# Performance work log

Measured on AMD Instinct MI355X. Metric: run time of the kernel, lower is better.

The kernel has to match this reference:

```python
import jax, jax.numpy as jnp
import numpy as np

NUM_NODES = 100000
EMB = 64
HID = 128
OUT = 64
N_EDGES = 1600000
N_LABEL = 200000


def setup_inputs() -> dict:
    key = jax.random.key(0)
    ks = jax.random.split(key, 8)
    return {
        "emb": jax.random.normal(ks[0], (NUM_NODES, EMB), jnp.float32) * 0.05,
        "w1l": jax.random.normal(ks[1], (HID, EMB), jnp.float32) * 0.05,
        "w1r": jax.random.normal(ks[2], (HID, EMB), jnp.float32) * 0.05,
        "b1": jnp.zeros((HID,), jnp.float32),
        "w2l": jax.random.normal(ks[3], (OUT, HID), jnp.float32) * 0.05,
        "w2r": jax.random.normal(ks[4], (OUT, HID), jnp.float32) * 0.05,
        "b2": jnp.zeros((OUT,), jnp.float32),
        "edge_index": jax.random.randint(ks[5], (2, N_EDGES), 0, NUM_NODES, jnp.int32),
        "edge_label_index": jax.random.randint(ks[6], (2, N_LABEL), 0, NUM_NODES, jnp.int32),
    }


def reference(emb, w1l, w1r, b1, w2l, w2r, b2, edge_index, edge_label_index):
    # PyG SAGEConv (aggr='mean'): out = mean_{j in N(i)} x_j @ W_l^T + b_l + x_i @ W_r^T
    n = emb.shape[0]
    src, dst = edge_index[0], edge_index[1]
    # in-degree per destination node, clamped to avoid div-by-zero (isolated nodes -> 0 agg)
    deg = jax.ops.segment_sum(jnp.ones(src.shape, emb.dtype), dst, num_segments=n)
    inv_deg = 1.0 / jnp.maximum(deg, 1.0)

    def sage(x, wl, wr, b):
        agg = jax.ops.segment_sum(x[src], dst, num_segments=n) * inv_deg[:, None]
        return agg @ wl.T + x @ wr.T + b

    h = jax.nn.relu(sage(emb, w1l, w1r, b1))  # dropout is identity in eval mode
    z = sage(h, w2l, w2r, b2)  # [N, OUT]
    # dot-product decode over candidate pairs
    return jnp.sum(z[edge_label_index[0]] * z[edge_label_index[1]], axis=-1)
```

## Files before the change

### kernel.cpp

```cpp
#include <hip/hip_runtime.h>

#define NN   100000
#define EMB  64
#define HID  128
#define OUTD 64
#define NE   1600000
#define NL   200000
#define NBUK 6250
#define NG   8
#define CAPG 128
#define BSTR 6272

typedef __attribute__((ext_vector_type(4))) float f32x4;
typedef __attribute__((ext_vector_type(8))) short s16x8;
typedef __attribute__((ext_vector_type(4))) unsigned short us4;

__device__ __forceinline__ unsigned short f2bf(float f) {
    unsigned u = __float_as_uint(f);
    u += 0x7FFFu + ((u >> 16) & 1u);
    return (unsigned short)(u >> 16);
}
__device__ __forceinline__ float bf2f(unsigned short h) {
    return __uint_as_float(((unsigned)h) << 16);
}

__device__ __forceinline__ unsigned xcc_id() {
    unsigned v;
    asm volatile("s_getreg_b32 %0, hwreg(HW_REG_XCC_ID)" : "=s"(v));
    return v & (NG - 1);
}

__global__ void bucket16_kernel(const int* __restrict__ src, const int* __restrict__ dst,
                                int* __restrict__ bcnt, int* __restrict__ tmp) {
    int i = blockIdx.x * blockDim.x + threadIdx.x;
    if (i >= NE / 4) return;
    unsigned g = xcc_id();
    int* cb = bcnt + g * BSTR;
    int4 d4 = ((const int4*)dst)[i];
    int4 s4 = ((const int4*)src)[i];
    int b0 = d4.x >> 4, b1 = d4.y >> 4, b2 = d4.z >> 4, b3 = d4.w >> 4;
    int p0 = atomicAdd(&cb[b0], 1);
    int p1 = atomicAdd(&cb[b1], 1);
    int p2 = atomicAdd(&cb[b2], 1);
    int p3 = atomicAdd(&cb[b3], 1);
    if (p0 < CAPG) tmp[((size_t)g * NBUK + b0) * CAPG + p0] = ((d4.x & 15) << 17) | s4.x;
    if (p1 < CAPG) tmp[((size_t)g * NBUK + b1) * CAPG + p1] = ((d4.y & 15) << 17) | s4.y;
    if (p2 < CAPG) tmp[((size_t)g * NBUK + b2) * CAPG + p2] = ((d4.z & 15) << 17) | s4.z;
    if (p3 < CAPG) tmp[((size_t)g * NBUK + b3) * CAPG + p3] = ((d4.w & 15) << 17) | s4.w;
}

__global__ void conv_emb_kernel(const float* __restrict__ emb, unsigned short* __restrict__ embb) {
    int i = blockIdx.x * blockDim.x + threadIdx.x;
    if (i >= NN * 16) return;
    float4 v = ((const float4*)emb)[i];
    us4 o;
    o.x = f2bf(v.x); o.y = f2bf(v.y); o.z = f2bf(v.z); o.w = f2bf(v.w);
    ((us4*)embb)[i] = o;
}

__global__ void conv_w_kernel(const float* __restrict__ w1l, const float* __restrict__ w1r,
                              const float* __restrict__ w2l, const float* __restrict__ w2r,
                              unsigned short* __restrict__ w1cat, unsigned short* __restrict__ w2cat) {
    int t = blockIdx.x * blockDim.x + threadIdx.x;
    if (t >= 128 * 128) return;
    int o = t >> 7, k = t & 127;
    w1cat[t] = f2bf(k < 64 ? w1l[o * 64 + k] : w1r[o * 64 + (k - 64)]);
    w2cat[t] = f2bf(o < 64 ? w2l[o * 128 + k] : w2r[(o - 64) * 128 + k]);
}

template<bool L1>
__global__ void __launch_bounds__(256) agg16_kernel(
        const int* __restrict__ bcnt, const int* __restrict__ tmp,
        const unsigned short* __restrict__ xb,
        const float* __restrict__ hz, const float* __restrict__ bias,
        unsigned short* __restrict__ outb, float* __restrict__ outf) {
    __shared__ int cgs[NG];
    __shared__ int goff[NG];
    __shared__ int total;
    __shared__ int scnt[16];
    __shared__ int soff[16];
    __shared__ int scur[16];
    __shared__ int plist[NG * CAPG];
    __shared__ int slist[NG * CAPG];

    const int b    = blockIdx.x;
    const int tid  = threadIdx.x;
    const int lane = tid & 63;
    const int wv   = tid >> 6;

    if (tid < NG) cgs[tid] = min(bcnt[tid * BSTR + b], CAPG);
    if (tid < 16) scnt[tid] = 0;
    __syncthreads();

    if (tid == 0) {
        int acc = 0;
#pragma unroll
        for (int g = 0; g < NG; ++g) { int c = cgs[g]; goff[g] = acc; acc += c; }
        total = acc;
    }
    __syncthreads();

    for (int t = tid; t < NG * CAPG; t += 256) {
        int g = t >> 7;
        int i = t & (CAPG - 1);
        if (i < cgs[g])
            plist[goff[g] + i] = tmp[((size_t)g * NBUK + b) * CAPG + i];
    }
    __syncthreads();

    const int cnt = total;
    for (int i = tid; i < cnt; i += 256)
        atomicAdd(&scnt[plist[i] >> 17], 1);
    __syncthreads();

    if (tid == 0) {
        int acc = 0;
#pragma unroll
        for (int r = 0; r < 16; ++r) {
            soff[r] = acc;
            scur[r] = acc;
            acc += scnt[r];
        }
    }
    __syncthreads();

    for (int i = tid; i < cnt; i += 256) {
        int p = plist[i];
        int pos = atomicAdd(&scur[p >> 17], 1);
        slist[pos] = p & 0x1FFFF;
    }
    __syncthreads();

#define LDX(c) bf2f(xb[(size_t)(c) * 64 + lane])
    for (int r = wv; r < 16; r += 4) {
        const int node = b * 16 + r;
        const int s = soff[r];
        const int d = scnt[r];
        float acc = 0.f;
        int j = 0;
        for (; j + 8 <= d; j += 8) {
            int c0 = slist[s + j + 0], c1 = slist[s + j + 1];
            int c2 = slist[s + j + 2], c3 = slist[s + j + 3];
            int c4 = slist[s + j + 4], c5 = slist[s + j + 5];
            int c6 = slist[s + j + 6], c7 = slist[s + j + 7];
            float v0 = LDX(c0), v1 = LDX(c1), v2 = LDX(c2), v3 = LDX(c3);
            float v4 = LDX(c4), v5 = LDX(c5), v6 = LDX(c6), v7 = LDX(c7);
            acc += ((v0 + v1) + (v2 + v3)) + ((v4 + v5) + (v6 + v7));
        }
        if (j + 4 <= d) {
            int c0 = slist[s + j + 0], c1 = slist[s + j + 1];
            int c2 = slist[s + j + 2], c3 = slist[s + j + 3];
            float v0 = LDX(c0), v1 = LDX(c1), v2 = LDX(c2), v3 = LDX(c3);
            acc += (v0 + v1) + (v2 + v3);
            j += 4;
        }
        for (; j < d; ++j) acc += LDX(slist[s + j]);

        const float inv = 1.0f / fmaxf((float)d, 1.0f);
        if (L1) {
            outb[(size_t)node * 64 + lane] = f2bf(acc * inv);
        } else {
            outf[(size_t)node * 64 + lane] =
                acc * inv + hz[(size_t)node * 64 + lane] + bias[lane];
        }
    }
#undef LDX
}

__global__ void __launch_bounds__(256) gemm_mfma_kernel(
        const unsigned short* __restrict__ aggb, const unsigned short* __restrict__ embb,
        const unsigned short* __restrict__ w1cat, const float* __restrict__ b1,
        const unsigned short* __restrict__ w2cat,
        unsigned short* __restrict__ p2b, float* __restrict__ hz) {
    __shared__ unsigned short h_lds[128 * 136];

    const int tid  = threadIdx.x;
    const int lane = tid & 63;
    const int w    = tid >> 6;
    const int l15  = lane & 15;
    const int lk   = lane >> 4;
    const int n_base = blockIdx.x * 128;
    const int mrow0  = w * 32;

    f32x4 acc[2][8];
#pragma unroll
    for (int mt = 0; mt < 2; ++mt)
#pragma unroll
        for (int nt = 0; nt < 8; ++nt) acc[mt][nt] = (f32x4)(0.f);

#pragma unroll
    for (int ks = 0; ks < 4; ++ks) {
        const int kc = ks * 32 + lk * 8;
        s16x8 a[2];
#pragma unroll
        for (int mt = 0; mt < 2; ++mt) {
            int n = n_base + mrow0 + mt * 16 + l15;
            s16x8 av = (s16x8)(short)0;
            if (n < NN) {
                const unsigned short* ap = (kc < 64)
                    ? (aggb + (size_t)n * 64 + kc)
                    : (embb + (size_t)n * 64 + (kc - 64));
                av = *(const s16x8*)ap;
            }
            a[mt] = av;
        }
#pragma unroll
        for (int nt = 0; nt < 8; ++nt) {
            s16x8 bv = *(const s16x8*)(w1cat + (nt * 16 + l15) * 128 + kc);
            acc[0][nt] = __builtin_amdgcn_mfma_f32_16x16x32_bf16(a[0], bv, acc[0][nt], 0, 0, 0);
            acc[1][nt] = __builtin_amdgcn_mfma_f32_16x16x32_bf16(a[1], bv, acc[1][nt], 0, 0, 0);
        }
    }

    float b1v[8];
#pragma unroll
    for (int nt = 0; nt < 8; ++nt) b1v[nt] = b1[nt * 16 + l15];
#pragma unroll
    for (int mt = 0; mt < 2; ++mt)
#pragma unroll
        for (int nt = 0; nt < 8; ++nt) {
            f32x4 d = acc[mt][nt];
            int o = nt * 16 + l15;
            int r0 = mrow0 + mt * 16 + lk * 4;
#pragma unroll
            for (int j = 0; j < 4; ++j)
                h_lds[(r0 + j) * 136 + o] = f2bf(fmaxf(d[j] + b1v[nt], 0.f));
        }

#pragma unroll
    for (int mt = 0; mt < 2; ++mt)
#pragma unroll
        for (int nt = 0; nt < 8; ++nt) acc[mt][nt] = (f32x4)(0.f);

#pragma unroll
    for (int ks = 0; ks < 4; ++ks) {
        const int kc = ks * 32 + lk * 8;
        s16x8 a[2];
#pragma unroll
        for (int mt = 0; mt < 2; ++mt)
            a[mt] = *(const s16x8*)&h_lds[(mrow0 + mt * 16 + l15) * 136 + kc];
#pragma unroll
        for (int nt = 0; nt < 8; ++nt) {
            s16x8 bv = *(const s16x8*)(w2cat + (nt * 16 + l15) * 128 + kc);
            acc[0][nt] = __builtin_amdgcn_mfma_f32_16x16x32_bf16(a[0], bv, acc[0][nt], 0, 0, 0);
            acc[1][nt] = __builtin_amdgcn_mfma_f32_16x16x32_bf16(a[1], bv, acc[1][nt], 0, 0, 0);
        }
    }

#pragma unroll
    for (int mt = 0; mt < 2; ++mt)
#pragma unroll
        for (int nt = 0; nt < 8; ++nt) {
            f32x4 d = acc[mt][nt];
            int o = nt * 16 + l15;
            int r0 = n_base + mrow0 + mt * 16 + lk * 4;
#pragma unroll
            for (int j = 0; j < 4; ++j) {
                int r = r0 + j;
                if (r >= NN) continue;
                if (nt < 4) p2b[(size_t)r * 64 + o] = f2bf(d[j]);
                else        hz[(size_t)r * 64 + (o - 64)] = d[j];
            }
        }
}

__global__ void decode_kernel(const int* __restrict__ a, const int* __restrict__ b,
                              const float* __restrict__ z, float* __restrict__ out) {
    int t = blockIdx.x * blockDim.x + threadIdx.x;
    int k = t >> 4;
    int q = t & 15;
    if (k >= NL) return;
    int ia = a[k], ib = b[k];
    float4 va = ((const float4*)z)[ia * 16 + q];
    float4 vb = ((const float4*)z)[ib * 16 + q];
    float s = va.x * vb.x + va.y * vb.y + va.z * vb.z + va.w * vb.w;
    s += __shfl_xor(s, 1, 64);
    s += __shfl_xor(s, 2, 64);
    s += __shfl_xor(s, 4, 64);
    s += __shfl_xor(s, 8, 64);
    if (q == 0) out[k] = s;
}

extern "C" void kernel_launch(void* const* d_in, const int* in_sizes, int n_in,
                              void* d_out, int out_size, void* d_ws, size_t ws_size,
                              hipStream_t stream) {
    const float* emb = (const float*)d_in[0];
    const float* w1l = (const float*)d_in[1];
    const float* w1r = (const float*)d_in[2];
    const float* b1  = (const float*)d_in[3];
    const float* w2l = (const float*)d_in[4];
    const float* w2r = (const float*)d_in[5];
    const float* b2  = (const float*)d_in[6];
    const int*   ei  = (const int*)d_in[7];
    const int*   eli = (const int*)d_in[8];
    float* out = (float*)d_out;

    int* bcnt = (int*)d_ws;
    int* tmp  = bcnt + NG * BSTR;
    unsigned short* aggb  = (unsigned short*)(tmp + (size_t)NG * NBUK * CAPG);
    unsigned short* embb  = aggb + (size_t)NN * 64;
    unsigned short* p2b   = embb + (size_t)NN * 64;
    unsigned short* w1cat = p2b + (size_t)NN * 64;
    unsigned short* w2cat = w1cat + 128 * 128;
    float* hz = (float*)(w2cat + 128 * 128);
    float* z  = hz + (size_t)NN * 64;

    const int* src = ei;
    const int* dst = ei + NE;

    hipMemsetAsync(bcnt, 0, (size_t)NG * BSTR * sizeof(int), stream);

    bucket16_kernel<<<(NE / 4 + 255) / 256, 256, 0, stream>>>(src, dst, bcnt, tmp);
    conv_emb_kernel<<<(NN * 16 + 255) / 256, 256, 0, stream>>>(emb, embb);
    conv_w_kernel<<<64, 256, 0, stream>>>(w1l, w1r, w2l, w2r, w1cat, w2cat);

    agg16_kernel<true><<<NBUK, 256, 0, stream>>>(bcnt, tmp, embb, nullptr, nullptr,
                                                 aggb, nullptr);

    const int NT = (NN + 127) / 128;
    gemm_mfma_kernel<<<NT, 256, 0, stream>>>(aggb, embb, w1cat, b1, w2cat, p2b, hz);

    agg16_kernel<false><<<NBUK, 256, 0, stream>>>(bcnt, tmp, p2b, hz, b2,
                                                  nullptr, z);

    decode_kernel<<<(NL * 16 + 255) / 256, 256, 0, stream>>>(eli, eli + NL, z, out);
}
```

Measured before the change: 237.2 us.

## Fuse prep kernels, store final z in bf16, use nontemporal loads

```diff
diff --git a/kernel.cpp b/kernel.cpp
--- a/kernel.cpp
+++ b/kernel.cpp
@@ -11,9 +11,14 @@
 #define CAPG 128
 #define BSTR 6272
 
+#define BUK_BLOCKS  1563
+#define CEMB_BLOCKS 400
+#define CW_BLOCKS   64
+
 typedef __attribute__((ext_vector_type(4))) float f32x4;
 typedef __attribute__((ext_vector_type(8))) short s16x8;
 typedef __attribute__((ext_vector_type(4))) unsigned short us4;
+typedef __attribute__((ext_vector_type(4))) int v4i;
 
 __device__ __forceinline__ unsigned short f2bf(float f) {
     unsigned u = __float_as_uint(f);
@@ -30,42 +35,46 @@
     return v & (NG - 1);
 }
 
-__global__ void bucket16_kernel(const int* __restrict__ src, const int* __restrict__ dst,
-                                int* __restrict__ bcnt, int* __restrict__ tmp) {
-    int i = blockIdx.x * blockDim.x + threadIdx.x;
-    if (i >= NE / 4) return;
-    unsigned g = xcc_id();
-    int* cb = bcnt + g * BSTR;
-    int4 d4 = ((const int4*)dst)[i];
-    int4 s4 = ((const int4*)src)[i];
-    int b0 = d4.x >> 4, b1 = d4.y >> 4, b2 = d4.z >> 4, b3 = d4.w >> 4;
-    int p0 = atomicAdd(&cb[b0], 1);
-    int p1 = atomicAdd(&cb[b1], 1);
-    int p2 = atomicAdd(&cb[b2], 1);
-    int p3 = atomicAdd(&cb[b3], 1);
-    if (p0 < CAPG) tmp[((size_t)g * NBUK + b0) * CAPG + p0] = ((d4.x & 15) << 17) | s4.x;
-    if (p1 < CAPG) tmp[((size_t)g * NBUK + b1) * CAPG + p1] = ((d4.y & 15) << 17) | s4.y;
-    if (p2 < CAPG) tmp[((size_t)g * NBUK + b2) * CAPG + p2] = ((d4.z & 15) << 17) | s4.z;
-    if (p3 < CAPG) tmp[((size_t)g * NBUK + b3) * CAPG + p3] = ((d4.w & 15) << 17) | s4.w;
-}
-
-__global__ void conv_emb_kernel(const float* __restrict__ emb, unsigned short* __restrict__ embb) {
-    int i = blockIdx.x * blockDim.x + threadIdx.x;
-    if (i >= NN * 16) return;
-    float4 v = ((const float4*)emb)[i];
-    us4 o;
-    o.x = f2bf(v.x); o.y = f2bf(v.y); o.z = f2bf(v.z); o.w = f2bf(v.w);
-    ((us4*)embb)[i] = o;
-}
-
-__global__ void conv_w_kernel(const float* __restrict__ w1l, const float* __restrict__ w1r,
-                              const float* __restrict__ w2l, const float* __restrict__ w2r,
-                              unsigned short* __restrict__ w1cat, unsigned short* __restrict__ w2cat) {
-    int t = blockIdx.x * blockDim.x + threadIdx.x;
-    if (t >= 128 * 128) return;
-    int o = t >> 7, k = t & 127;
-    w1cat[t] = f2bf(k < 64 ? w1l[o * 64 + k] : w1r[o * 64 + (k - 64)]);
-    w2cat[t] = f2bf(o < 64 ? w2l[o * 128 + k] : w2r[(o - 64) * 128 + k]);
+__global__ void __launch_bounds__(256) prep_kernel(
+        const int* __restrict__ src, const int* __restrict__ dst,
+        int* __restrict__ bcnt, int* __restrict__ tmp,
+        const float* __restrict__ emb, unsigned short* __restrict__ embb,
+        const float* __restrict__ w1l, const float* __restrict__ w1r,
+        const float* __restrict__ w2l, const float* __restrict__ w2r,
+        unsigned short* __restrict__ w1cat, unsigned short* __restrict__ w2cat) {
+    const int bid = blockIdx.x;
+    const int tid = threadIdx.x;
+
+    if (bid < BUK_BLOCKS) {
+        int i = bid * 256 + tid;
+        if (i >= NE / 4) return;
+        unsigned g = xcc_id();
+        int* cb = bcnt + g * BSTR;
+        v4i d4 = __builtin_nontemporal_load((const v4i*)dst + i);
+        v4i s4 = __builtin_nontemporal_load((const v4i*)src + i);
+        int b0 = d4[0] >> 4, b1 = d4[1] >> 4, b2 = d4[2] >> 4, b3 = d4[3] >> 4;
+        int p0 = atomicAdd(&cb[b0], 1);
+        int p1 = atomicAdd(&cb[b1], 1);
+        int p2 = atomicAdd(&cb[b2], 1);
+        int p3 = atomicAdd(&cb[b3], 1);
+        if (p0 < CAPG) tmp[((size_t)g * NBUK + b0) * CAPG + p0] = ((d4[0] & 15) << 17) | s4[0];
+        if (p1 < CAPG) tmp[((size_t)g * NBUK + b1) * CAPG + p1] = ((d4[1] & 15) << 17) | s4[1];
+        if (p2 < CAPG) tmp[((size_t)g * NBUK + b2) * CAPG + p2] = ((d4[2] & 15) << 17) | s4[2];
+        if (p3 < CAPG) tmp[((size_t)g * NBUK + b3) * CAPG + p3] = ((d4[3] & 15) << 17) | s4[3];
+    } else if (bid < BUK_BLOCKS + CEMB_BLOCKS) {
+        for (int i = (bid - BUK_BLOCKS) * 256 + tid; i < NN * 16; i += CEMB_BLOCKS * 256) {
+            float4 v = ((const float4*)emb)[i];
+            us4 o;
+            o.x = f2bf(v.x); o.y = f2bf(v.y); o.z = f2bf(v.z); o.w = f2bf(v.w);
+            ((us4*)embb)[i] = o;
+        }
+    } else {
+        int t = (bid - BUK_BLOCKS - CEMB_BLOCKS) * 256 + tid;
+        if (t >= 128 * 128) return;
+        int o = t >> 7, k = t & 127;
+        w1cat[t] = f2bf(k < 64 ? w1l[o * 64 + k] : w1r[o * 64 + (k - 64)]);
+        w2cat[t] = f2bf(o < 64 ? w2l[o * 128 + k] : w2r[(o - 64) * 128 + k]);
+    }
 }
 
 template<bool L1>
@@ -73,7 +82,7 @@
         const int* __restrict__ bcnt, const int* __restrict__ tmp,
         const unsigned short* __restrict__ xb,
         const float* __restrict__ hz, const float* __restrict__ bias,
-        unsigned short* __restrict__ outb, float* __restrict__ outf) {
+        unsigned short* __restrict__ outb) {
     __shared__ int cgs[NG];
     __shared__ int goff[NG];
     __shared__ int total;
@@ -104,7 +113,8 @@
         int g = t >> 7;
         int i = t & (CAPG - 1);
         if (i < cgs[g])
-            plist[goff[g] + i] = tmp[((size_t)g * NBUK + b) * CAPG + i];
+            plist[goff[g] + i] = __builtin_nontemporal_load(
+                tmp + ((size_t)g * NBUK + b) * CAPG + i);
     }
     __syncthreads();
 
@@ -160,8 +170,8 @@
         if (L1) {
             outb[(size_t)node * 64 + lane] = f2bf(acc * inv);
         } else {
-            outf[(size_t)node * 64 + lane] =
-                acc * inv + hz[(size_t)node * 64 + lane] + bias[lane];
+            outb[(size_t)node * 64 + lane] =
+                f2bf(acc * inv + hz[(size_t)node * 64 + lane] + bias[lane]);
         }
     }
 #undef LDX
@@ -265,15 +275,16 @@
 }
 
 __global__ void decode_kernel(const int* __restrict__ a, const int* __restrict__ b,
-                              const float* __restrict__ z, float* __restrict__ out) {
+                              const unsigned short* __restrict__ zb, float* __restrict__ out) {
     int t = blockIdx.x * blockDim.x + threadIdx.x;
     int k = t >> 4;
     int q = t & 15;
     if (k >= NL) return;
     int ia = a[k], ib = b[k];
-    float4 va = ((const float4*)z)[ia * 16 + q];
-    float4 vb = ((const float4*)z)[ib * 16 + q];
-    float s = va.x * vb.x + va.y * vb.y + va.z * vb.z + va.w * vb.w;
+    us4 va = ((const us4*)zb)[ia * 16 + q];
+    us4 vb = ((const us4*)zb)[ib * 16 + q];
+    float s = bf2f(va.x) * bf2f(vb.x) + bf2f(va.y) * bf2f(vb.y)
+            + bf2f(va.z) * bf2f(vb.z) + bf2f(va.w) * bf2f(vb.w);
     s += __shfl_xor(s, 1, 64);
     s += __shfl_xor(s, 2, 64);
     s += __shfl_xor(s, 4, 64);
@@ -300,28 +311,25 @@
     unsigned short* aggb  = (unsigned short*)(tmp + (size_t)NG * NBUK * CAPG);
     unsigned short* embb  = aggb + (size_t)NN * 64;
     unsigned short* p2b   = embb + (size_t)NN * 64;
-    unsigned short* w1cat = p2b + (size_t)NN * 64;
+    unsigned short* zb    = p2b + (size_t)NN * 64;
+    unsigned short* w1cat = zb + (size_t)NN * 64;
     unsigned short* w2cat = w1cat + 128 * 128;
     float* hz = (float*)(w2cat + 128 * 128);
-    float* z  = hz + (size_t)NN * 64;
 
     const int* src = ei;
     const int* dst = ei + NE;
 
     hipMemsetAsync(bcnt, 0, (size_t)NG * BSTR * sizeof(int), stream);
 
-    bucket16_kernel<<<(NE / 4 + 255) / 256, 256, 0, stream>>>(src, dst, bcnt, tmp);
-    conv_emb_kernel<<<(NN * 16 + 255) / 256, 256, 0, stream>>>(emb, embb);
-    conv_w_kernel<<<64, 256, 0, stream>>>(w1l, w1r, w2l, w2r, w1cat, w2cat);
-
-    agg16_kernel<true><<<NBUK, 256, 0, stream>>>(bcnt, tmp, embb, nullptr, nullptr,
-                                                 aggb, nullptr);
+    prep_kernel<<<BUK_BLOCKS + CEMB_BLOCKS + CW_BLOCKS, 256, 0, stream>>>(
+        src, dst, bcnt, tmp, emb, embb, w1l, w1r, w2l, w2r, w1cat, w2cat);
+
+    agg16_kernel<true><<<NBUK, 256, 0, stream>>>(bcnt, tmp, embb, nullptr, nullptr, aggb);
 
     const int NT = (NN + 127) / 128;
     gemm_mfma_kernel<<<NT, 256, 0, stream>>>(aggb, embb, w1cat, b1, w2cat, p2b, hz);
 
-    agg16_kernel<false><<<NBUK, 256, 0, stream>>>(bcnt, tmp, p2b, hz, b2,
-                                                  nullptr, z);
-
-    decode_kernel<<<(NL * 16 + 255) / 256, 256, 0, stream>>>(eli, eli + NL, z, out);
-}
+    agg16_kernel<false><<<NBUK, 256, 0, stream>>>(bcnt, tmp, p2b, hz, b2, zb);
+
+    decode_kernel<<<(NL * 16 + 255) / 256, 256, 0, stream>>>(eli, eli + NL, zb, out);
+}
```

After: 233.8 us. No clear change (-1.5%).
